# Optimization experiments

Hardware: AMD Instinct MI355X
Metric: run time of the kernel (lower is better)

The kernel has to match this reference:

```python
import jax, jax.numpy as jnp
import numpy as np

HW, B, C, NH, NC, HF, WF = 2500, 2, 256, 8, 6, 64, 176
DFF = 4 * C
EPS = 1e-5

def _layernorm(x, g, b):
    m = x.mean(-1, keepdims=True)
    v = ((x - m) ** 2).mean(-1, keepdims=True)
    return (x - m) / jnp.sqrt(v + EPS) * g + b

def _mha(q, kv, in_w, in_b, ow, ob):
    # q: [L,B,C], kv: [S,B,C] (batch_first=False, torch nn.MultiheadAttention)
    L, Bq, Cq = q.shape
    S = kv.shape[0]
    Dh = Cq // NH
    qp = (q @ in_w[:Cq].T + in_b[:Cq]).reshape(L, Bq, NH, Dh)
    kp = (kv @ in_w[Cq:2 * Cq].T + in_b[Cq:2 * Cq]).reshape(S, Bq, NH, Dh)
    vp = (kv @ in_w[2 * Cq:].T + in_b[2 * Cq:]).reshape(S, Bq, NH, Dh)
    att = jnp.einsum('lbhd,sbhd->bhls', qp, kp) * (1.0 / np.sqrt(Dh))
    att = jax.nn.softmax(att, axis=-1)
    out = jnp.einsum('bhls,sbhd->lbhd', att, vp).reshape(L, Bq, Cq)
    return out @ ow.T + ob

def _grid_sample_zeros(feat, grid):
    # feat: [B,N,C,H,W], grid: [B,N,Q,2] in [-1,1]; bilinear, align_corners=False, zero padding
    Bb, N, Cc, Hf, Wf = feat.shape
    Q = grid.shape[2]
    x = (grid[..., 0] + 1.0) * (Wf / 2.0) - 0.5
    y = (grid[..., 1] + 1.0) * (Hf / 2.0) - 0.5
    x0 = jnp.floor(x); y0 = jnp.floor(y)
    wx = x - x0; wy = y - y0
    x0i = x0.astype(jnp.int32); y0i = y0.astype(jnp.int32)
    ff = feat.reshape(Bb, N, Cc, Hf * Wf)
    def corner(xi, yi, w):
        valid = (xi >= 0) & (xi < Wf) & (yi >= 0) & (yi < Hf)
        idx = jnp.clip(yi, 0, Hf - 1) * Wf + jnp.clip(xi, 0, Wf - 1)  # [B,N,Q]
        g = jnp.take_along_axis(ff, jnp.broadcast_to(idx[:, :, None, :], (Bb, N, Cc, Q)), axis=-1)
        return g * (w * valid)[:, :, None, :]
    return (corner(x0i, y0i, (1.0 - wx) * (1.0 - wy)) + corner(x0i + 1, y0i, wx * (1.0 - wy))
            + corner(x0i, y0i + 1, (1.0 - wx) * wy) + corner(x0i + 1, y0i + 1, wx * wy))

def _forward(bev_queries, prev_bev, image_feat, reference_points, camera_intrinsics, camera_extrinsics,
             in_proj_w, in_proj_b, out_proj_w, out_proj_b, tsa_norm_g, tsa_norm_b,
             sca_w, sca_b, sca_norm_g, sca_norm_b, ffn_w1, ffn_b1, ffn_w2, ffn_b2, ffn_norm_g, ffn_norm_b):
    # TSA (dropout is identity in eval)
    tsa_out = _mha(bev_queries, prev_bev, in_proj_w, in_proj_b, out_proj_w, out_proj_b)
    x = _layernorm(bev_queries + tsa_out, tsa_norm_g, tsa_norm_b)
    # SCA: ego->camera->image projection
    R = camera_extrinsics[:, :, :3, :3]            # [B,N,3,3]
    t = camera_extrinsics[:, :, :3, 3]             # [B,N,3]
    R_e2c = jnp.swapaxes(R, -1, -2)
    t_e2c = -jnp.einsum('bnij,bnj->bni', R_e2c, t)
    pts_cam = jnp.einsum('bnij,qj->bnqi', R_e2c, reference_points) + t_e2c[:, :, None, :]  # [B,N,Q,3]
    pts_img = jnp.einsum('bnij,bnqj->bnqi', camera_intrinsics, pts_cam)
    uv = pts_img[..., :2] / jnp.maximum(pts_img[..., 2:3], 1e-5)
    grid = jnp.stack([2.0 * uv[..., 0] / WF - 1.0, 2.0 * uv[..., 1] / HF - 1.0], axis=-1)  # [B,N,Q,2]
    Bq = bev_queries.shape[1]
    feat_r = image_feat.reshape(Bq, NC, C, HF, WF)
    sampled = _grid_sample_zeros(feat_r, grid).mean(axis=1)   # [B,C,Q]
    sampled = jnp.transpose(sampled, (2, 0, 1))               # [Q,B,C]
    sca_out = sampled @ sca_w.T + sca_b
    x = _layernorm(x + sca_out, sca_norm_g, sca_norm_b)
    # FFN (torch nn.GELU default = exact erf)
    h = jax.nn.gelu(x @ ffn_w1 + ffn_b1, approximate=False)
    ffn_out = h @ ffn_w2 + ffn_b2
    return _layernorm(x + ffn_out, ffn_norm_g, ffn_norm_b)

def setup_inputs():
    key = jax.random.key(0)
    ks = jax.random.split(key, 16)
    f = jnp.float32
    s = 0.02
    return {
        'bev_queries': jax.random.normal(ks[0], (HW, B, C), f),
        'prev_bev': jax.random.normal(ks[1], (HW, B, C), f),
        'image_feat': jax.random.normal(ks[2], (B * NC, C, HF, WF), f),
        'reference_points': jax.random.normal(ks[3], (HW, 3), f) * 20.0,
        'camera_intrinsics': jax.random.normal(ks[4], (B, NC, 3, 3), f),
        'camera_extrinsics': jax.random.normal(ks[5], (B, NC, 4, 4), f),
        'spatial_shapes': jnp.array([[HF, WF]], jnp.int32),
        'in_proj_w': jax.random.normal(ks[6], (3 * C, C), f) * s,
        'in_proj_b': jnp.zeros((3 * C,), f),
        'out_proj_w': jax.random.normal(ks[7], (C, C), f) * s,
        'out_proj_b': jnp.zeros((C,), f),
        'tsa_norm_g': jnp.ones((C,), f), 'tsa_norm_b': jnp.zeros((C,), f),
        'sca_w': jax.random.normal(ks[8], (C, C), f) * s,
        'sca_b': jnp.zeros((C,), f),
        'sca_norm_g': jnp.ones((C,), f), 'sca_norm_b': jnp.zeros((C,), f),
        'ffn_w1': jax.random.normal(ks[9], (C, DFF), f) * s,
        'ffn_b1': jnp.zeros((DFF,), f),
        'ffn_w2': jax.random.normal(ks[10], (DFF, C), f) * s,
        'ffn_b2': jnp.zeros((C,), f),
        'ffn_norm_g': jnp.ones((C,), f), 'ffn_norm_b': jnp.zeros((C,), f),
    }

def reference(bev_queries, prev_bev, image_feat, reference_points, camera_intrinsics, camera_extrinsics,
              in_proj_w, in_proj_b, out_proj_w, out_proj_b, tsa_norm_g, tsa_norm_b,
              sca_w, sca_b, sca_norm_g, sca_norm_b, ffn_w1, ffn_b1, ffn_w2, ffn_b2, ffn_norm_g, ffn_norm_b,
              spatial_shapes):
    return _forward(bev_queries, prev_bev, image_feat, reference_points, camera_intrinsics, camera_extrinsics,
                    in_proj_w, in_proj_b, out_proj_w, out_proj_b, tsa_norm_g, tsa_norm_b,
                    sca_w, sca_b, sca_norm_g, sca_norm_b, ffn_w1, ffn_b1, ffn_w2, ffn_b2, ffn_norm_g, ffn_norm_b)
```

## Files before the change

kernel.cpp:

```cpp
#include <hip/hip_runtime.h>

typedef unsigned short u16;
typedef __attribute__((ext_vector_type(8))) __bf16 bf8_t;
typedef __attribute__((ext_vector_type(4))) float f4_t;

union bf8u { u16 u[8]; bf8_t v; uint4 q; };

__device__ __forceinline__ float bf2f(u16 v) {
  return __uint_as_float(((unsigned int)v) << 16);
}
__device__ __forceinline__ u16 f2bf(float f) {
  union { __bf16 h; u16 u; } c;
  c.h = (__bf16)f;
  return c.u;
}
__device__ __forceinline__ float bflo(unsigned int w) { return __uint_as_float(w << 16); }
__device__ __forceinline__ float bfhi(unsigned int w) { return __uint_as_float(w & 0xFFFF0000u); }
__device__ __forceinline__ float ldf1(const void* p, size_t i, int isf32) {
  return isf32 ? ((const float*)p)[i] : bf2f(((const u16*)p)[i]);
}

#define LQ    2500
#define LQP   2560
#define BB    2
#define CC    256
#define NCC   6
#define HFF   64
#define WFF   176
#define DFF   1024
#define MROWS 5000

#define WB_UV   256
#define WB_WQKV 240256
#define WB_WOP  633472
#define WB_WSC  764544
#define WB_WF1  895616
#define WB_WF2  1419904
#define WB_S1   1944192
#define WB_S2   (WB_S1 + 2621440)
#define WB_S3   (WB_S2 + 2621440)
#define WB_VT   (WB_S3 + 2621440)
#define WB_H    WB_S2
#define WB_Y3   (WB_S2 + 10485760)

__global__ void detect_k(const u16* __restrict__ rp, int* __restrict__ flag) {
  int bad = 0;
  for (int i = threadIdx.x; i < 7500; i += 64) {
    float v = bf2f(rp[i]);
    if (!(fabsf(v) < 1e6f)) bad = 1;
  }
  int anybad = __any(bad);
  if (threadIdx.x == 0) flag[0] = anybad ? 1 : 0;
}

struct WDesc {
  const void* src[6];
  u16* dst[6];
  int n[6];
  int mode[6];
  int Kd[6], Nd[6];
};
__global__ __launch_bounds__(256) void cvtw_k(WDesc d, const int* __restrict__ flag) {
  const int df = flag[0];
  const int i = blockIdx.y;
  const int n = d.n[i];
  for (int j = blockIdx.x * 256 + threadIdx.x; j < n; j += gridDim.x * 256) {
    if (d.mode[i] == 2) {
      const int row = j / (LQP - LQ), col = LQ + j % (LQP - LQ);
      d.dst[i][(size_t)row * LQP + col] = 0;
    } else if (d.mode[i] == 1) {
      const int K = d.Kd[i], N = d.Nd[i];
      const int nn = j / K, kk = j - nn * K;
      d.dst[i][j] = f2bf(ldf1(d.src[i], (size_t)kk * N + nn, df));
    } else {
      d.dst[i][j] = f2bf(ldf1(d.src[i], j, df));
    }
  }
}

template<int KTPL, int XRAW, int ACT, int RES, int STORE_T, int NT>
__global__ __launch_bounds__(64) void gemm_nl(
    const void* __restrict__ Xv, const u16* __restrict__ W,
    const void* __restrict__ bias, size_t boff,
    const void* __restrict__ resv,
    u16* __restrict__ Y, int M, int N, const int* __restrict__ flag)
{
  const int df = flag[0];
  const int lane = threadIdx.x;
  const int ln15 = lane & 15, l4 = lane >> 4;
  const int m0 = blockIdx.x * 16, n0 = blockIdx.y * (NT * 16);
  const int am = min(m0 + ln15, M - 1);

  f4_t acc[NT];
#pragma unroll
  for (int nt = 0; nt < NT; ++nt) acc[nt] = (f4_t){0.f, 0.f, 0.f, 0.f};

#pragma unroll 8
  for (int k0 = 0; k0 < KTPL; k0 += 32) {
    bf8u a;
    if (XRAW && df) {
      const float* p = (const float*)Xv + (size_t)am * KTPL + k0 + l4 * 8;
      float4 r0 = *(const float4*)p, r1 = *(const float4*)(p + 4);
      a.u[0]=f2bf(r0.x); a.u[1]=f2bf(r0.y); a.u[2]=f2bf(r0.z); a.u[3]=f2bf(r0.w);
      a.u[4]=f2bf(r1.x); a.u[5]=f2bf(r1.y); a.u[6]=f2bf(r1.z); a.u[7]=f2bf(r1.w);
    } else {
      a.q = *(const uint4*)((const u16*)Xv + (size_t)am * KTPL + k0 + l4 * 8);
    }
#pragma unroll
    for (int nt = 0; nt < NT; ++nt) {
      bf8u b;
      b.q = *(const uint4*)&W[(size_t)(n0 + nt * 16 + ln15) * KTPL + k0 + l4 * 8];
      acc[nt] = __builtin_amdgcn_mfma_f32_16x16x32_bf16(a.v, b.v, acc[nt], 0, 0, 0);
    }
  }
#pragma unroll
  for (int nt = 0; nt < NT; ++nt) {
    const int gn = n0 + nt * 16 + ln15;
    const float bv = ldf1(bias, boff + gn, df);
#pragma unroll
    for (int r = 0; r < 4; ++r) {
      const int gm = m0 + l4 * 4 + r;
      if (gm < M) {
        float x = acc[nt][r] + bv;
        if (ACT) x = 0.5f * x * (1.f + erff(x * 0.70710678118654752f));
        if (RES == 1)      x += bf2f(((const u16*)resv)[(size_t)gm * N + gn]);
        else if (RES == 2) x += ldf1(resv, (size_t)gm * N + gn, df);
        if (STORE_T) {
          const int tt = gm >> 1;
          const int tx = tt & 63;
          const int tp = (tx & 35) | ((tx & 12) << 1) | ((tx & 16) >> 2);
          Y[(size_t)(gn + (gm & 1) * 256) * LQP + ((tt & ~63) | tp)] = f2bf(x);
        } else {
          Y[(size_t)gm * N + gn] = f2bf(x);
        }
      }
    }
  }
}

__global__ __launch_bounds__(64) void gemm_qkv(
    const void* __restrict__ Xq, const void* __restrict__ Xkv,
    const u16* __restrict__ Wqkv, const void* __restrict__ bias,
    u16* __restrict__ Qo, u16* __restrict__ Ko, u16* __restrict__ Vt,
    const int* __restrict__ flag)
{
  const int df = flag[0];
  const int lane = threadIdx.x;
  const int ln15 = lane & 15, l4 = lane >> 4;
  const int which = blockIdx.y >> 2;
  const int n0 = (blockIdx.y & 3) * 64;
  const void* Xv = (which == 0) ? Xq : Xkv;
  const u16* W = Wqkv + (size_t)which * 65536;
  const int m0 = blockIdx.x * 16;
  const int am = min(m0 + ln15, MROWS - 1);

  f4_t acc[4];
#pragma unroll
  for (int nt = 0; nt < 4; ++nt) acc[nt] = (f4_t){0.f, 0.f, 0.f, 0.f};

#pragma unroll 8
  for (int k0 = 0; k0 < CC; k0 += 32) {
    bf8u a;
    if (df) {
      const float* p = (const float*)Xv + (size_t)am * CC + k0 + l4 * 8;
      float4 r0 = *(const float4*)p, r1 = *(const float4*)(p + 4);
      a.u[0]=f2bf(r0.x); a.u[1]=f2bf(r0.y); a.u[2]=f2bf(r0.z); a.u[3]=f2bf(r0.w);
      a.u[4]=f2bf(r1.x); a.u[5]=f2bf(r1.y); a.u[6]=f2bf(r1.z); a.u[7]=f2bf(r1.w);
    } else {
      a.q = *(const uint4*)((const u16*)Xv + (size_t)am * CC + k0 + l4 * 8);
    }
#pragma unroll
    for (int nt = 0; nt < 4; ++nt) {
      bf8u b;
      b.q = *(const uint4*)&W[(size_t)(n0 + nt * 16 + ln15) * CC + k0 + l4 * 8];
      acc[nt] = __builtin_amdgcn_mfma_f32_16x16x32_bf16(a.v, b.v, acc[nt], 0, 0, 0);
    }
  }
#pragma unroll
  for (int nt = 0; nt < 4; ++nt) {
    const int gn = n0 + nt * 16 + ln15;
    const float bv = ldf1(bias, which * 256 + gn, df);
#pragma unroll
    for (int r = 0; r < 4; ++r) {
      const int gm = m0 + l4 * 4 + r;
      if (gm < MROWS) {
        const float x = acc[nt][r] + bv;
        if (which == 2) {
          const int tt = gm >> 1;
          const int tx = tt & 63;
          const int tp = (tx & 35) | ((tx & 12) << 1) | ((tx & 16) >> 2);
          Vt[(size_t)(gn + (gm & 1) * 256) * LQP + ((tt & ~63) | tp)] = f2bf(x);
        } else {
          u16* Y = (which == 0) ? Qo : Ko;
          Y[(size_t)gm * CC + gn] = f2bf(x);
        }
      }
    }
  }
}

#define TPW 10
__global__ __launch_bounds__(256) void attn_mf(
    const u16* __restrict__ Qw, const u16* __restrict__ Kw,
    const u16* __restrict__ Vt, u16* __restrict__ Ow)
{
  __shared__ float sO[4][16][33];
  __shared__ float sM[4][16];
  __shared__ float sL[4][16];
  const int t = threadIdx.x;
  const int lane = t & 63, w = t >> 6;
  const int ln15 = lane & 15, l4 = lane >> 4;
  const int q0 = blockIdx.x * 16;
  const int by = blockIdx.y;
  const int b = by >> 3, h = by & 7;
  const float SCL2E = 0.25505654481f;

  bf8u aq;
  {
    const int qrow = min(q0 + ln15, LQ - 1);
    bf8u qr; qr.q = *(const uint4*)&Qw[((size_t)qrow * BB + b) * CC + h * 32 + l4 * 8];
#pragma unroll
    for (int i = 0; i < 8; ++i) aq.u[i] = f2bf(bf2f(qr.u[i]) * SCL2E);
  }

  f4_t oacc[2];
  oacc[0] = (f4_t){0.f,0.f,0.f,0.f};
  oacc[1] = (f4_t){0.f,0.f,0.f,0.f};
  float m_r = -1e30f;
  float l_r = 0.f;

  const int kt0 = w * TPW;
  const u16* Kbase = &Kw[(size_t)b * CC + h * 32 + l4 * 8];
  const u16* Vbase = &Vt[(size_t)(by * 32 + ln15) * LQP + l4 * 8];

  bf8u bkn[4];
#pragma unroll
  for (int nt = 0; nt < 4; ++nt)
    bkn[nt].q = *(const uint4*)&Kbase[(size_t)(kt0 * 64 + nt * 16 + ln15) * CC];

  for (int kt = kt0; kt < kt0 + TPW; ++kt) {
    const int kb = kt * 64;
    bf8u av[2][2];
#pragma unroll
    for (int m = 0; m < 2; ++m)
#pragma unroll
      for (int dt = 0; dt < 2; ++dt)
        av[m][dt].q = *(const uint4*)&Vbase[(size_t)(dt * 16) * LQP + kb + m * 32];
    bf8u bk[4];
#pragma unroll
    for (int nt = 0; nt < 4; ++nt) bk[nt] = bkn[nt];
    if (kt + 1 < kt0 + TPW) {
#pragma unroll
      for (int nt = 0; nt < 4; ++nt)
        bkn[nt].q = *(const uint4*)&Kbase[(size_t)(kb + 64 + nt * 16 + ln15) * CC];
    }
    f4_t sv[4];
    __builtin_amdgcn_s_setprio(1);
#pragma unroll
    for (int nt = 0; nt < 4; ++nt) {
      f4_t z = (f4_t){0.f,0.f,0.f,0.f};
      sv[nt] = __builtin_amdgcn_mfma_f32_16x16x32_bf16(bk[nt].v, aq.v, z, 0, 0, 0);
    }
    __builtin_amdgcn_s_setprio(0);
    float p[4][4];
    if (kb + 64 <= LQ) {
#pragma unroll
      for (int nt = 0; nt < 4; ++nt)
#pragma unroll
        for (int r = 0; r < 4; ++r) p[nt][r] = sv[nt][r];
    } else {
#pragma unroll
      for (int nt = 0; nt < 4; ++nt)
#pragma unroll
        for (int r = 0; r < 4; ++r)
          p[nt][r] = (kb + nt * 16 + l4 * 4 + r < LQ) ? sv[nt][r] : -1e30f;
    }
    const float m0 = fmaxf(fmaxf(p[0][0], p[0][1]), fmaxf(p[0][2], p[0][3]));
    const float m1 = fmaxf(fmaxf(p[1][0], p[1][1]), fmaxf(p[1][2], p[1][3]));
    const float m2 = fmaxf(fmaxf(p[2][0], p[2][1]), fmaxf(p[2][2], p[2][3]));
    const float m3 = fmaxf(fmaxf(p[3][0], p[3][1]), fmaxf(p[3][2], p[3][3]));
    float mloc = fmaxf(fmaxf(m0, m1), fmaxf(m2, m3));
    mloc = fmaxf(mloc, __shfl_xor(mloc, 16));
    mloc = fmaxf(mloc, __shfl_xor(mloc, 32));
    if (__any(mloc > m_r + 8.f)) {
      const float mn = fmaxf(m_r, mloc);
      const float alpha = __builtin_amdgcn_exp2f(m_r - mn);
      m_r = mn;
      l_r *= alpha;
#pragma unroll
      for (int r = 0; r < 4; ++r) { oacc[0][r] *= alpha; oacc[1][r] *= alpha; }
    }
    float s = 0.f;
#pragma unroll
    for (int nt = 0; nt < 4; ++nt) {
#pragma unroll
      for (int r = 0; r < 4; ++r) {
        const float e = __builtin_amdgcn_exp2f(p[nt][r] - m_r);
        p[nt][r] = e; s += e;
      }
    }
    l_r += s;
    __builtin_amdgcn_s_setprio(1);
#pragma unroll
    for (int m = 0; m < 2; ++m) {
      bf8u pb;
#pragma unroll
      for (int i = 0; i < 8; ++i) pb.u[i] = f2bf(p[2 * m + (i >> 2)][i & 3]);
#pragma unroll
      for (int dt = 0; dt < 2; ++dt)
        oacc[dt] = __builtin_amdgcn_mfma_f32_16x16x32_bf16(av[m][dt].v, pb.v, oacc[dt], 0, 0, 0);
    }
    __builtin_amdgcn_s_setprio(0);
  }
  l_r += __shfl_xor(l_r, 16);
  l_r += __shfl_xor(l_r, 32);
#pragma unroll
  for (int dt = 0; dt < 2; ++dt)
#pragma unroll
    for (int r = 0; r < 4; ++r)
      sO[w][ln15][dt * 16 + l4 * 4 + r] = oacc[dt][r];
  if (l4 == 0) { sM[w][ln15] = m_r; sL[w][ln15] = l_r; }
  __syncthreads();
#pragma unroll
  for (int i = t; i < 512; i += 256) {
    const int row = i >> 5, col = i & 31;
    const float M = fmaxf(fmaxf(sM[0][row], sM[1][row]), fmaxf(sM[2][row], sM[3][row]));
    float l = 0.f, O = 0.f;
#pragma unroll
    for (int w4 = 0; w4 < 4; ++w4) {
      const float sc = __builtin_amdgcn_exp2f(sM[w4][row] - M);
      l += sc * sL[w4][row];
      O += sc * sO[w4][row][col];
    }
    const int q = q0 + row;
    if (q < LQ)
      Ow[((size_t)q * BB + b) * CC + h * 32 + col] = f2bf(O / l);
  }
}

template<int TOOUT>
__global__ __launch_bounds__(256) void ln_k(const u16* __restrict__ X,
    const void* __restrict__ g, const void* __restrict__ be,
    void* __restrict__ Yv, int rows, const int* __restrict__ flag)
{
  const int df = flag[0];
  const int lane = threadIdx.x & 63;
  const int row = blockIdx.x * 4 + (threadIdx.x >> 6);
  if (row >= rows) return;
  uint2 raw = *(const uint2*)(X + (size_t)row * CC + lane * 4);
  float vx = bflo(raw.x), vy = bfhi(raw.x), vz = bflo(raw.y), vw = bfhi(raw.y);
  float s = vx + vy + vz + vw;
#pragma unroll
  for (int o = 1; o < 64; o <<= 1) s += __shfl_xor(s, o);
  const float mean = s * 0.00390625f;
  const float dx = vx - mean, dy = vy - mean, dz = vz - mean, dw = vw - mean;
  float sq = dx*dx + dy*dy + dz*dz + dw*dw;
#pragma unroll
  for (int o = 1; o < 64; o <<= 1) sq += __shfl_xor(sq, o);
  const float rstd = rsqrtf(sq * 0.00390625f + 1e-5f);
  const float g0 = ldf1(g, lane*4+0, df), g1 = ldf1(g, lane*4+1, df);
  const float g2 = ldf1(g, lane*4+2, df), g3 = ldf1(g, lane*4+3, df);
  const float b0 = ldf1(be, lane*4+0, df), b1 = ldf1(be, lane*4+1, df);
  const float b2 = ldf1(be, lane*4+2, df), b3 = ldf1(be, lane*4+3, df);
  const float y0 = dx * rstd * g0 + b0;
  const float y1 = dy * rstd * g1 + b1;
  const float y2 = dz * rstd * g2 + b2;
  const float y3 = dw * rstd * g3 + b3;
  if (TOOUT && df) {
    float* yp = (float*)Yv + (size_t)row * CC + lane * 4;
    *(float4*)yp = make_float4(y0, y1, y2, y3);
  } else {
    u16* yp = (u16*)Yv + (size_t)row * CC + lane * 4;
    unsigned int lo = (unsigned int)f2bf(y0) | ((unsigned int)f2bf(y1) << 16);
    unsigned int hi = (unsigned int)f2bf(y2) | ((unsigned int)f2bf(y3) << 16);
    *(uint2*)yp = make_uint2(lo, hi);
  }
}

__global__ __launch_bounds__(256) void uv_k(
    const void* __restrict__ refp, const void* __restrict__ intr,
    const void* __restrict__ extr, float* __restrict__ uv,
    const int* __restrict__ flag)
{
  const int df = flag[0];
  const int idx = blockIdx.x * 256 + threadIdx.x;
  if (idx >= BB * NCC * LQ) return;
  const int bc = idx / LQ;
  const int q = idx - bc * LQ;
  float R[3][3], tv[3], Kc[3][3], p[3];
#pragma unroll
  for (int i = 0; i < 3; ++i) {
#pragma unroll
    for (int j = 0; j < 3; ++j) {
      R[i][j] = ldf1(extr, bc*16 + i*4 + j, df);
      Kc[i][j] = ldf1(intr, bc*9 + i*3 + j, df);
    }
    tv[i] = ldf1(extr, bc*16 + i*4 + 3, df);
  }
#pragma unroll
  for (int j = 0; j < 3; ++j) p[j] = ldf1(refp, q*3 + j, df) - tv[j];
  float pc[3];
#pragma unroll
  for (int i = 0; i < 3; ++i) pc[i] = R[0][i]*p[0] + R[1][i]*p[1] + R[2][i]*p[2];
  float im[3];
#pragma unroll
  for (int i = 0; i < 3; ++i) im[i] = Kc[i][0]*pc[0] + Kc[i][1]*pc[1] + Kc[i][2]*pc[2];
  const float z = fmaxf(im[2], 1e-5f);
  uv[(size_t)idx*2 + 0] = im[0] / z - 0.5f;
  uv[(size_t)idx*2 + 1] = im[1] / z - 0.5f;
}

__global__ __launch_bounds__(256) void samp_k(
    const void* __restrict__ feat, const float* __restrict__ uv,
    u16* __restrict__ S, const int* __restrict__ flag)
{
  const int df = flag[0];
  const int c = blockIdx.x;
  const int b = blockIdx.y / 5;
  const int ch = blockIdx.y % 5;
  const int qend = min((ch + 1) * 500, LQ);
  for (int q = ch * 500 + threadIdx.x; q < qend; q += 256) {
    float acc = 0.f;
#pragma unroll
    for (int cam = 0; cam < NCC; ++cam) {
      const int bc = b * NCC + cam;
      const float x = uv[((size_t)bc * LQ + q) * 2 + 0];
      const float y = uv[((size_t)bc * LQ + q) * 2 + 1];
      const float xf = floorf(x), yf = floorf(y);
      const int x0 = (int)xf, y0 = (int)yf;
      const float wx = x - xf, wy = y - yf;
      const size_t base = ((size_t)bc * CC + c) * (HFF * WFF);
      const bool vx0 = (x0 >= 0) & (x0 < WFF);
      const bool vx1 = (x0 + 1 >= 0) & (x0 + 1 < WFF);
      const bool vy0 = (y0 >= 0) & (y0 < HFF);
      const bool vy1 = (y0 + 1 >= 0) & (y0 + 1 < HFF);
      if (vy0) {
        const size_t rb = base + (size_t)y0 * WFF;
        if (vx0) acc += (1.f - wx) * (1.f - wy) * ldf1(feat, rb + x0, df);
        if (vx1) acc += wx * (1.f - wy) * ldf1(feat, rb + x0 + 1, df);
      }
      if (vy1) {
        const size_t rb = base + (size_t)(y0 + 1) * WFF;
        if (vx0) acc += (1.f - wx) * wy * ldf1(feat, rb + x0, df);
        if (vx1) acc += wx * wy * ldf1(feat, rb + x0 + 1, df);
      }
    }
    S[((size_t)q * BB + b) * CC + c] = f2bf(acc * (1.f / 6.f));
  }
}

extern "C" void kernel_launch(void* const* d_in, const int* in_sizes, int n_in,
                              void* d_out, int out_size, void* d_ws, size_t ws_size,
                              hipStream_t stream) {
  (void)in_sizes; (void)n_in; (void)out_size; (void)ws_size;
  char* base = (char*)d_ws;
  int* flag = (int*)base;
  float* UV = (float*)(base + WB_UV);
  u16* WQKV = (u16*)(base + WB_WQKV);
  u16* WOP  = (u16*)(base + WB_WOP);
  u16* WSC  = (u16*)(base + WB_WSC);
  u16* WF1  = (u16*)(base + WB_WF1);
  u16* WF2  = (u16*)(base + WB_WF2);
  u16* S1 = (u16*)(base + WB_S1);
  u16* S2 = (u16*)(base + WB_S2);
  u16* S3 = (u16*)(base + WB_S3);
  u16* VT = (u16*)(base + WB_VT);
  u16* H  = (u16*)(base + WB_H);
  u16* Y3 = (u16*)(base + WB_Y3);

  detect_k<<<1, 64, 0, stream>>>((const u16*)d_in[3], flag);

  WDesc wd;
  wd.src[0] = d_in[7];  wd.dst[0] = WQKV; wd.n[0] = 196608; wd.mode[0] = 0; wd.Kd[0] = 0;    wd.Nd[0] = 0;
  wd.src[1] = d_in[9];  wd.dst[1] = WOP;  wd.n[1] = 65536;  wd.mode[1] = 0; wd.Kd[1] = 0;    wd.Nd[1] = 0;
  wd.src[2] = d_in[13]; wd.dst[2] = WSC;  wd.n[2] = 65536;  wd.mode[2] = 0; wd.Kd[2] = 0;    wd.Nd[2] = 0;
  wd.src[3] = d_in[17]; wd.dst[3] = WF1;  wd.n[3] = 262144; wd.mode[3] = 1; wd.Kd[3] = 256;  wd.Nd[3] = 1024;
  wd.src[4] = d_in[19]; wd.dst[4] = WF2;  wd.n[4] = 262144; wd.mode[4] = 1; wd.Kd[4] = 1024; wd.Nd[4] = 256;
  wd.src[5] = nullptr;  wd.dst[5] = VT;   wd.n[5] = 512 * (LQP - LQ); wd.mode[5] = 2; wd.Kd[5] = 0; wd.Nd[5] = 0;
  cvtw_k<<<dim3(128, 6), 256, 0, stream>>>(wd, flag);

  uv_k<<<(BB * NCC * LQ + 255) / 256, 256, 0, stream>>>(d_in[3], d_in[4], d_in[5], UV, flag);

  gemm_qkv<<<dim3(313, 12), 64, 0, stream>>>(d_in[0], d_in[1], WQKV, d_in[8], S1, S2, VT, flag);

  attn_mf<<<dim3(157, 16), 256, 0, stream>>>(S1, S2, VT, S3);

  gemm_nl<256,0,0,2,0,1><<<dim3(313, 16), 64, 0, stream>>>(S3, WOP, d_in[10], 0, d_in[0], S1, MROWS, CC, flag);
  ln_k<0><<<1250, 256, 0, stream>>>(S1, d_in[11], d_in[12], S2, MROWS, flag);

  samp_k<<<dim3(CC, BB * 5), 256, 0, stream>>>(d_in[2], UV, VT, flag);

  gemm_nl<256,0,0,1,0,1><<<dim3(313, 16), 64, 0, stream>>>(VT, WSC, d_in[14], 0, S2, S3, MROWS, CC, flag);
  ln_k<0><<<1250, 256, 0, stream>>>(S3, d_in[15], d_in[16], S1, MROWS, flag);

  gemm_nl<256,0,1,0,0,4><<<dim3(313, 16), 64, 0, stream>>>(S1, WF1, d_in[18], 0, nullptr, H,  MROWS, DFF, flag);
  gemm_nl<1024,0,0,1,0,1><<<dim3(313, 16), 64, 0, stream>>>(H,  WF2, d_in[20], 0, S1,      Y3, MROWS, CC,  flag);
  ln_k<1><<<1250, 256, 0, stream>>>(Y3, d_in[21], d_in[22], d_out, MROWS, flag);
}
```

Baseline: 519.7 us.

## Stage camera feature planes in LDS for sampling and widen GEMM N-tiles

The sampling kernel now loads each 64x176 feature plane for a (channel, camera) into shared memory, converting bf16 to float once, then samples all queries from LDS. Each thread keeps ten per-query accumulators across the six cameras, so the grid drops from 10 to 2 blocks per channel. This removes scattered global gathers at the cost of 44KB of LDS per block and lower occupancy. Three N=256 GEMMs also switch to a template setting that covers four times as many output columns per block, cutting grid.y from 16 to 4.

```diff
diff --git a/kernel.cpp b/kernel.cpp
--- a/kernel.cpp
+++ b/kernel.cpp
@@ -414,38 +414,71 @@
     const void* __restrict__ feat, const float* __restrict__ uv,
     u16* __restrict__ S, const int* __restrict__ flag)
 {
+  __shared__ float pl[HFF * WFF];
   const int df = flag[0];
   const int c = blockIdx.x;
-  const int b = blockIdx.y / 5;
-  const int ch = blockIdx.y % 5;
-  const int qend = min((ch + 1) * 500, LQ);
-  for (int q = ch * 500 + threadIdx.x; q < qend; q += 256) {
-    float acc = 0.f;
-#pragma unroll
-    for (int cam = 0; cam < NCC; ++cam) {
-      const int bc = b * NCC + cam;
-      const float x = uv[((size_t)bc * LQ + q) * 2 + 0];
-      const float y = uv[((size_t)bc * LQ + q) * 2 + 1];
-      const float xf = floorf(x), yf = floorf(y);
-      const int x0 = (int)xf, y0 = (int)yf;
-      const float wx = x - xf, wy = y - yf;
-      const size_t base = ((size_t)bc * CC + c) * (HFF * WFF);
-      const bool vx0 = (x0 >= 0) & (x0 < WFF);
-      const bool vx1 = (x0 + 1 >= 0) & (x0 + 1 < WFF);
-      const bool vy0 = (y0 >= 0) & (y0 < HFF);
-      const bool vy1 = (y0 + 1 >= 0) & (y0 + 1 < HFF);
-      if (vy0) {
-        const size_t rb = base + (size_t)y0 * WFF;
-        if (vx0) acc += (1.f - wx) * (1.f - wy) * ldf1(feat, rb + x0, df);
-        if (vx1) acc += wx * (1.f - wy) * ldf1(feat, rb + x0 + 1, df);
+  const int b = blockIdx.y;
+  const int t = threadIdx.x;
+
+  float acc[10];
+#pragma unroll
+  for (int j = 0; j < 10; ++j) acc[j] = 0.f;
+
+  for (int cam = 0; cam < NCC; ++cam) {
+    const int bc = b * NCC + cam;
+    const size_t base = ((size_t)bc * CC + c) * (HFF * WFF);
+    __syncthreads();
+    if (df) {
+      const float4* src = (const float4*)((const float*)feat + base);
+#pragma unroll
+      for (int i = 0; i < 11; ++i) {
+        const int g = i * 256 + t;
+        *(float4*)&pl[g * 4] = src[g];
       }
-      if (vy1) {
-        const size_t rb = base + (size_t)(y0 + 1) * WFF;
-        if (vx0) acc += (1.f - wx) * wy * ldf1(feat, rb + x0, df);
-        if (vx1) acc += wx * wy * ldf1(feat, rb + x0 + 1, df);
+    } else {
+      const uint2* src = (const uint2*)((const u16*)feat + base);
+#pragma unroll
+      for (int i = 0; i < 11; ++i) {
+        const int g = i * 256 + t;
+        const uint2 r = src[g];
+        *(float4*)&pl[g * 4] = make_float4(bflo(r.x), bfhi(r.x), bflo(r.y), bfhi(r.y));
       }
     }
-    S[((size_t)q * BB + b) * CC + c] = f2bf(acc * (1.f / 6.f));
+    __syncthreads();
+    const float* uvb = &uv[(size_t)bc * LQ * 2];
+#pragma unroll
+    for (int j = 0; j < 10; ++j) {
+      const int q = j * 256 + t;
+      if (q < LQ) {
+        const float x = uvb[q * 2 + 0];
+        const float y = uvb[q * 2 + 1];
+        const float xf = floorf(x), yf = floorf(y);
+        const int x0 = (int)xf, y0 = (int)yf;
+        const float wx = x - xf, wy = y - yf;
+        const bool vx0 = (x0 >= 0) & (x0 < WFF);
+        const bool vx1 = (x0 + 1 >= 0) & (x0 + 1 < WFF);
+        const bool vy0 = (y0 >= 0) & (y0 < HFF);
+        const bool vy1 = (y0 + 1 >= 0) & (y0 + 1 < HFF);
+        float a = 0.f;
+        if (vy0) {
+          const int rb = y0 * WFF;
+          if (vx0) a += (1.f - wx) * (1.f - wy) * pl[rb + x0];
+          if (vx1) a += wx * (1.f - wy) * pl[rb + x0 + 1];
+        }
+        if (vy1) {
+          const int rb = (y0 + 1) * WFF;
+          if (vx0) a += (1.f - wx) * wy * pl[rb + x0];
+          if (vx1) a += wx * wy * pl[rb + x0 + 1];
+        }
+        acc[j] += a;
+      }
+    }
+  }
+#pragma unroll
+  for (int j = 0; j < 10; ++j) {
+    const int q = j * 256 + t;
+    if (q < LQ)
+      S[((size_t)q * BB + b) * CC + c] = f2bf(acc[j] * (1.f / 6.f));
   }
 }
 
@@ -485,15 +518,15 @@
 
   attn_mf<<<dim3(157, 16), 256, 0, stream>>>(S1, S2, VT, S3);
 
-  gemm_nl<256,0,0,2,0,1><<<dim3(313, 16), 64, 0, stream>>>(S3, WOP, d_in[10], 0, d_in[0], S1, MROWS, CC, flag);
+  gemm_nl<256,0,0,2,0,4><<<dim3(313, 4), 64, 0, stream>>>(S3, WOP, d_in[10], 0, d_in[0], S1, MROWS, CC, flag);
   ln_k<0><<<1250, 256, 0, stream>>>(S1, d_in[11], d_in[12], S2, MROWS, flag);
 
-  samp_k<<<dim3(CC, BB * 5), 256, 0, stream>>>(d_in[2], UV, VT, flag);
-
-  gemm_nl<256,0,0,1,0,1><<<dim3(313, 16), 64, 0, stream>>>(VT, WSC, d_in[14], 0, S2, S3, MROWS, CC, flag);
+  samp_k<<<dim3(CC, BB), 256, 0, stream>>>(d_in[2], UV, VT, flag);
+
+  gemm_nl<256,0,0,1,0,4><<<dim3(313, 4), 64, 0, stream>>>(VT, WSC, d_in[14], 0, S2, S3, MROWS, CC, flag);
   ln_k<0><<<1250, 256, 0, stream>>>(S3, d_in[15], d_in[16], S1, MROWS, flag);
 
   gemm_nl<256,0,1,0,0,4><<<dim3(313, 16), 64, 0, stream>>>(S1, WF1, d_in[18], 0, nullptr, H,  MROWS, DFF, flag);
-  gemm_nl<1024,0,0,1,0,1><<<dim3(313, 16), 64, 0, stream>>>(H,  WF2, d_in[20], 0, S1,      Y3, MROWS, CC,  flag);
+  gemm_nl<1024,0,0,1,0,4><<<dim3(313, 4),  64, 0, stream>>>(H,  WF2, d_in[20], 0, S1,      Y3, MROWS, CC,  flag);
   ln_k<1><<<1250, 256, 0, stream>>>(Y3, d_in[21], d_in[22], d_out, MROWS, flag);
 }
```

Measured after the change: 517.0 us. No clear change (-0.5%).

## Fuse layernorm into output GEMMs, merge uv projection into weight conversion

Applied to the files above, without the earlier changes.

Adds a gemm_ln kernel in which four waves each compute 64 output columns of a 16-row tile, add bias and residual, and apply layernorm through shared-memory row reductions. It replaces three GEMM plus ln_k pairs, which removes three launches and the write and re-read of the pre-norm intermediates. The uv camera projection now runs as an extra grid row of the weight conversion kernel, the plain weight copies are vectorised to four elements per thread, and the attention rescale check skips the max reduction when no element passes the threshold. A cost is that each output GEMM now launches 313 blocks instead of 5008, which lowers parallelism across CUs.

```diff
diff --git a/kernel.cpp b/kernel.cpp
--- a/kernel.cpp
+++ b/kernel.cpp
@@ -41,7 +41,6 @@
 #define WB_S3   (WB_S2 + 2621440)
 #define WB_VT   (WB_S3 + 2621440)
 #define WB_H    WB_S2
-#define WB_Y3   (WB_S2 + 10485760)
 
 __global__ void detect_k(const u16* __restrict__ rp, int* __restrict__ flag) {
   int bad = 0;
@@ -60,29 +59,66 @@
   int mode[6];
   int Kd[6], Nd[6];
 };
-__global__ __launch_bounds__(256) void cvtw_k(WDesc d, const int* __restrict__ flag) {
+__global__ __launch_bounds__(256) void cvtw_k(WDesc d,
+    const void* __restrict__ refp, const void* __restrict__ intr,
+    const void* __restrict__ extr, float* __restrict__ uv,
+    const int* __restrict__ flag) {
   const int df = flag[0];
   const int i = blockIdx.y;
+  if (i == 6) {
+    for (int idx = blockIdx.x * 256 + threadIdx.x; idx < BB * NCC * LQ; idx += gridDim.x * 256) {
+      const int bc = idx / LQ;
+      const int q = idx - bc * LQ;
+      float R[3][3], tv[3], Kc[3][3], p[3];
+#pragma unroll
+      for (int a = 0; a < 3; ++a) {
+#pragma unroll
+        for (int j = 0; j < 3; ++j) {
+          R[a][j] = ldf1(extr, bc*16 + a*4 + j, df);
+          Kc[a][j] = ldf1(intr, bc*9 + a*3 + j, df);
+        }
+        tv[a] = ldf1(extr, bc*16 + a*4 + 3, df);
+      }
+#pragma unroll
+      for (int j = 0; j < 3; ++j) p[j] = ldf1(refp, q*3 + j, df) - tv[j];
+      float pc[3];
+#pragma unroll
+      for (int a = 0; a < 3; ++a) pc[a] = R[0][a]*p[0] + R[1][a]*p[1] + R[2][a]*p[2];
+      float im[3];
+#pragma unroll
+      for (int a = 0; a < 3; ++a) im[a] = Kc[a][0]*pc[0] + Kc[a][1]*pc[1] + Kc[a][2]*pc[2];
+      const float z = fmaxf(im[2], 1e-5f);
+      uv[(size_t)idx*2 + 0] = im[0] / z - 0.5f;
+      uv[(size_t)idx*2 + 1] = im[1] / z - 0.5f;
+    }
+    return;
+  }
   const int n = d.n[i];
   for (int j = blockIdx.x * 256 + threadIdx.x; j < n; j += gridDim.x * 256) {
-    if (d.mode[i] == 2) {
+    if (d.mode[i] == 3) {
+      if (df) {
+        const float4 r = ((const float4*)d.src[i])[j];
+        const unsigned int lo = (unsigned int)f2bf(r.x) | ((unsigned int)f2bf(r.y) << 16);
+        const unsigned int hi = (unsigned int)f2bf(r.z) | ((unsigned int)f2bf(r.w) << 16);
+        ((uint2*)d.dst[i])[j] = make_uint2(lo, hi);
+      } else {
+        ((uint2*)d.dst[i])[j] = ((const uint2*)d.src[i])[j];
+      }
+    } else if (d.mode[i] == 2) {
       const int row = j / (LQP - LQ), col = LQ + j % (LQP - LQ);
       d.dst[i][(size_t)row * LQP + col] = 0;
-    } else if (d.mode[i] == 1) {
+    } else {
       const int K = d.Kd[i], N = d.Nd[i];
       const int nn = j / K, kk = j - nn * K;
       d.dst[i][j] = f2bf(ldf1(d.src[i], (size_t)kk * N + nn, df));
-    } else {
-      d.dst[i][j] = f2bf(ldf1(d.src[i], j, df));
-    }
-  }
-}
-
-template<int KTPL, int XRAW, int ACT, int RES, int STORE_T, int NT>
+    }
+  }
+}
+
+template<int KTPL, int ACT, int NT>
 __global__ __launch_bounds__(64) void gemm_nl(
-    const void* __restrict__ Xv, const u16* __restrict__ W,
-    const void* __restrict__ bias, size_t boff,
-    const void* __restrict__ resv,
+    const u16* __restrict__ Xv, const u16* __restrict__ W,
+    const void* __restrict__ bias,
     u16* __restrict__ Y, int M, int N, const int* __restrict__ flag)
 {
   const int df = flag[0];
@@ -98,14 +134,7 @@
 #pragma unroll 8
   for (int k0 = 0; k0 < KTPL; k0 += 32) {
     bf8u a;
-    if (XRAW && df) {
-      const float* p = (const float*)Xv + (size_t)am * KTPL + k0 + l4 * 8;
-      float4 r0 = *(const float4*)p, r1 = *(const float4*)(p + 4);
-      a.u[0]=f2bf(r0.x); a.u[1]=f2bf(r0.y); a.u[2]=f2bf(r0.z); a.u[3]=f2bf(r0.w);
-      a.u[4]=f2bf(r1.x); a.u[5]=f2bf(r1.y); a.u[6]=f2bf(r1.z); a.u[7]=f2bf(r1.w);
-    } else {
-      a.q = *(const uint4*)((const u16*)Xv + (size_t)am * KTPL + k0 + l4 * 8);
-    }
+    a.q = *(const uint4*)(Xv + (size_t)am * KTPL + k0 + l4 * 8);
 #pragma unroll
     for (int nt = 0; nt < NT; ++nt) {
       bf8u b;
@@ -116,23 +145,116 @@
 #pragma unroll
   for (int nt = 0; nt < NT; ++nt) {
     const int gn = n0 + nt * 16 + ln15;
-    const float bv = ldf1(bias, boff + gn, df);
+    const float bv = ldf1(bias, gn, df);
 #pragma unroll
     for (int r = 0; r < 4; ++r) {
       const int gm = m0 + l4 * 4 + r;
       if (gm < M) {
         float x = acc[nt][r] + bv;
         if (ACT) x = 0.5f * x * (1.f + erff(x * 0.70710678118654752f));
-        if (RES == 1)      x += bf2f(((const u16*)resv)[(size_t)gm * N + gn]);
-        else if (RES == 2) x += ldf1(resv, (size_t)gm * N + gn, df);
-        if (STORE_T) {
-          const int tt = gm >> 1;
-          const int tx = tt & 63;
-          const int tp = (tx & 35) | ((tx & 12) << 1) | ((tx & 16) >> 2);
-          Y[(size_t)(gn + (gm & 1) * 256) * LQP + ((tt & ~63) | tp)] = f2bf(x);
-        } else {
-          Y[(size_t)gm * N + gn] = f2bf(x);
-        }
+        Y[(size_t)gm * N + gn] = f2bf(x);
+      }
+    }
+  }
+}
+
+template<int KT, int RES, int TOOUT>
+__global__ __launch_bounds__(256) void gemm_ln(
+    const u16* __restrict__ Xv, const u16* __restrict__ W,
+    const void* __restrict__ bias, const void* __restrict__ resv,
+    const void* __restrict__ gw, const void* __restrict__ bw,
+    void* __restrict__ Yv, int M, const int* __restrict__ flag)
+{
+  __shared__ float sR[4][16];
+  const int df = flag[0];
+  const int t = threadIdx.x;
+  const int lane = t & 63, wn = t >> 6;
+  const int ln15 = lane & 15, l4 = lane >> 4;
+  const int m0 = blockIdx.x * 16;
+  const int am = min(m0 + ln15, M - 1);
+
+  f4_t acc[4];
+#pragma unroll
+  for (int nt = 0; nt < 4; ++nt) acc[nt] = (f4_t){0.f, 0.f, 0.f, 0.f};
+
+#pragma unroll 8
+  for (int k0 = 0; k0 < KT; k0 += 32) {
+    bf8u a;
+    a.q = *(const uint4*)(Xv + (size_t)am * KT + k0 + l4 * 8);
+#pragma unroll
+    for (int nt = 0; nt < 4; ++nt) {
+      bf8u b;
+      b.q = *(const uint4*)&W[(size_t)(wn * 64 + nt * 16 + ln15) * KT + k0 + l4 * 8];
+      acc[nt] = __builtin_amdgcn_mfma_f32_16x16x32_bf16(a.v, b.v, acc[nt], 0, 0, 0);
+    }
+  }
+  float x[4][4];
+#pragma unroll
+  for (int nt = 0; nt < 4; ++nt) {
+    const int gn = wn * 64 + nt * 16 + ln15;
+    const float bv = ldf1(bias, gn, df);
+#pragma unroll
+    for (int r = 0; r < 4; ++r) {
+      const int gm = m0 + l4 * 4 + r;
+      float xx = acc[nt][r] + bv;
+      const size_t ri = (size_t)min(gm, M - 1) * CC + gn;
+      if (RES == 1)      xx += bf2f(((const u16*)resv)[ri]);
+      else if (RES == 2) xx += ldf1(resv, ri, df);
+      x[nt][r] = xx;
+    }
+  }
+  float ps[4];
+#pragma unroll
+  for (int r = 0; r < 4; ++r) {
+    ps[r] = x[0][r] + x[1][r] + x[2][r] + x[3][r];
+#pragma unroll
+    for (int o = 1; o < 16; o <<= 1) ps[r] += __shfl_xor(ps[r], o);
+  }
+  if (ln15 == 0) {
+#pragma unroll
+    for (int r = 0; r < 4; ++r) sR[wn][l4 * 4 + r] = ps[r];
+  }
+  __syncthreads();
+  float mean[4];
+#pragma unroll
+  for (int r = 0; r < 4; ++r) {
+    const int row = l4 * 4 + r;
+    mean[r] = (sR[0][row] + sR[1][row] + sR[2][row] + sR[3][row]) * 0.00390625f;
+  }
+  __syncthreads();
+  float pq[4];
+#pragma unroll
+  for (int r = 0; r < 4; ++r) {
+    float d0 = x[0][r] - mean[r], d1 = x[1][r] - mean[r];
+    float d2 = x[2][r] - mean[r], d3 = x[3][r] - mean[r];
+    pq[r] = d0*d0 + d1*d1 + d2*d2 + d3*d3;
+#pragma unroll
+    for (int o = 1; o < 16; o <<= 1) pq[r] += __shfl_xor(pq[r], o);
+  }
+  if (ln15 == 0) {
+#pragma unroll
+    for (int r = 0; r < 4; ++r) sR[wn][l4 * 4 + r] = pq[r];
+  }
+  __syncthreads();
+  float rstd[4];
+#pragma unroll
+  for (int r = 0; r < 4; ++r) {
+    const int row = l4 * 4 + r;
+    const float v = (sR[0][row] + sR[1][row] + sR[2][row] + sR[3][row]) * 0.00390625f;
+    rstd[r] = rsqrtf(v + 1e-5f);
+  }
+#pragma unroll
+  for (int nt = 0; nt < 4; ++nt) {
+    const int gn = wn * 64 + nt * 16 + ln15;
+    const float g = ldf1(gw, gn, df);
+    const float be = ldf1(bw, gn, df);
+#pragma unroll
+    for (int r = 0; r < 4; ++r) {
+      const int gm = m0 + l4 * 4 + r;
+      if (gm < M) {
+        const float y = (x[nt][r] - mean[r]) * rstd[r] * g + be;
+        if (TOOUT && df) ((float*)Yv)[(size_t)gm * CC + gn] = y;
+        else             ((u16*)Yv)[(size_t)gm * CC + gn] = f2bf(y);
       }
     }
   }
@@ -275,14 +397,20 @@
         for (int r = 0; r < 4; ++r)
           p[nt][r] = (kb + nt * 16 + l4 * 4 + r < LQ) ? sv[nt][r] : -1e30f;
     }
-    const float m0 = fmaxf(fmaxf(p[0][0], p[0][1]), fmaxf(p[0][2], p[0][3]));
-    const float m1 = fmaxf(fmaxf(p[1][0], p[1][1]), fmaxf(p[1][2], p[1][3]));
-    const float m2 = fmaxf(fmaxf(p[2][0], p[2][1]), fmaxf(p[2][2], p[2][3]));
-    const float m3 = fmaxf(fmaxf(p[3][0], p[3][1]), fmaxf(p[3][2], p[3][3]));
-    float mloc = fmaxf(fmaxf(m0, m1), fmaxf(m2, m3));
-    mloc = fmaxf(mloc, __shfl_xor(mloc, 16));
-    mloc = fmaxf(mloc, __shfl_xor(mloc, 32));
-    if (__any(mloc > m_r + 8.f)) {
+    const float thr = m_r + 8.f;
+    bool nd = false;
+#pragma unroll
+    for (int nt = 0; nt < 4; ++nt)
+#pragma unroll
+      for (int r = 0; r < 4; ++r) nd |= (p[nt][r] > thr);
+    if (__any(nd)) {
+      const float m0 = fmaxf(fmaxf(p[0][0], p[0][1]), fmaxf(p[0][2], p[0][3]));
+      const float m1 = fmaxf(fmaxf(p[1][0], p[1][1]), fmaxf(p[1][2], p[1][3]));
+      const float m2 = fmaxf(fmaxf(p[2][0], p[2][1]), fmaxf(p[2][2], p[2][3]));
+      const float m3 = fmaxf(fmaxf(p[3][0], p[3][1]), fmaxf(p[3][2], p[3][3]));
+      float mloc = fmaxf(fmaxf(m0, m1), fmaxf(m2, m3));
+      mloc = fmaxf(mloc, __shfl_xor(mloc, 16));
+      mloc = fmaxf(mloc, __shfl_xor(mloc, 32));
       const float mn = fmaxf(m_r, mloc);
       const float alpha = __builtin_amdgcn_exp2f(m_r - mn);
       m_r = mn;
@@ -336,78 +464,6 @@
     if (q < LQ)
       Ow[((size_t)q * BB + b) * CC + h * 32 + col] = f2bf(O / l);
   }
-}
-
-template<int TOOUT>
-__global__ __launch_bounds__(256) void ln_k(const u16* __restrict__ X,
-    const void* __restrict__ g, const void* __restrict__ be,
-    void* __restrict__ Yv, int rows, const int* __restrict__ flag)
-{
-  const int df = flag[0];
-  const int lane = threadIdx.x & 63;
-  const int row = blockIdx.x * 4 + (threadIdx.x >> 6);
-  if (row >= rows) return;
-  uint2 raw = *(const uint2*)(X + (size_t)row * CC + lane * 4);
-  float vx = bflo(raw.x), vy = bfhi(raw.x), vz = bflo(raw.y), vw = bfhi(raw.y);
-  float s = vx + vy + vz + vw;
-#pragma unroll
-  for (int o = 1; o < 64; o <<= 1) s += __shfl_xor(s, o);
-  const float mean = s * 0.00390625f;
-  const float dx = vx - mean, dy = vy - mean, dz = vz - mean, dw = vw - mean;
-  float sq = dx*dx + dy*dy + dz*dz + dw*dw;
-#pragma unroll
-  for (int o = 1; o < 64; o <<= 1) sq += __shfl_xor(sq, o);
-  const float rstd = rsqrtf(sq * 0.00390625f + 1e-5f);
-  const float g0 = ldf1(g, lane*4+0, df), g1 = ldf1(g, lane*4+1, df);
-  const float g2 = ldf1(g, lane*4+2, df), g3 = ldf1(g, lane*4+3, df);
-  const float b0 = ldf1(be, lane*4+0, df), b1 = ldf1(be, lane*4+1, df);
-  const float b2 = ldf1(be, lane*4+2, df), b3 = ldf1(be, lane*4+3, df);
-  const float y0 = dx * rstd * g0 + b0;
-  const float y1 = dy * rstd * g1 + b1;
-  const float y2 = dz * rstd * g2 + b2;
-  const float y3 = dw * rstd * g3 + b3;
-  if (TOOUT && df) {
-    float* yp = (float*)Yv + (size_t)row * CC + lane * 4;
-    *(float4*)yp = make_float4(y0, y1, y2, y3);
-  } else {
-    u16* yp = (u16*)Yv + (size_t)row * CC + lane * 4;
-    unsigned int lo = (unsigned int)f2bf(y0) | ((unsigned int)f2bf(y1) << 16);
-    unsigned int hi = (unsigned int)f2bf(y2) | ((unsigned int)f2bf(y3) << 16);
-    *(uint2*)yp = make_uint2(lo, hi);
-  }
-}
-
-__global__ __launch_bounds__(256) void uv_k(
-    const void* __restrict__ refp, const void* __restrict__ intr,
-    const void* __restrict__ extr, float* __restrict__ uv,
-    const int* __restrict__ flag)
-{
-  const int df = flag[0];
-  const int idx = blockIdx.x * 256 + threadIdx.x;
-  if (idx >= BB * NCC * LQ) return;
-  const int bc = idx / LQ;
-  const int q = idx - bc * LQ;
-  float R[3][3], tv[3], Kc[3][3], p[3];
-#pragma unroll
-  for (int i = 0; i < 3; ++i) {
-#pragma unroll
-    for (int j = 0; j < 3; ++j) {
-      R[i][j] = ldf1(extr, bc*16 + i*4 + j, df);
-      Kc[i][j] = ldf1(intr, bc*9 + i*3 + j, df);
-    }
-    tv[i] = ldf1(extr, bc*16 + i*4 + 3, df);
-  }
-#pragma unroll
-  for (int j = 0; j < 3; ++j) p[j] = ldf1(refp, q*3 + j, df) - tv[j];
-  float pc[3];
-#pragma unroll
-  for (int i = 0; i < 3; ++i) pc[i] = R[0][i]*p[0] + R[1][i]*p[1] + R[2][i]*p[2];
-  float im[3];
-#pragma unroll
-  for (int i = 0; i < 3; ++i) im[i] = Kc[i][0]*pc[0] + Kc[i][1]*pc[1] + Kc[i][2]*pc[2];
-  const float z = fmaxf(im[2], 1e-5f);
-  uv[(size_t)idx*2 + 0] = im[0] / z - 0.5f;
-  uv[(size_t)idx*2 + 1] = im[1] / z - 0.5f;
 }
 
 __global__ __launch_bounds__(256) void samp_k(
@@ -466,34 +522,28 @@
   u16* S3 = (u16*)(base + WB_S3);
   u16* VT = (u16*)(base + WB_VT);
   u16* H  = (u16*)(base + WB_H);
-  u16* Y3 = (u16*)(base + WB_Y3);
 
   detect_k<<<1, 64, 0, stream>>>((const u16*)d_in[3], flag);
 
   WDesc wd;
-  wd.src[0] = d_in[7];  wd.dst[0] = WQKV; wd.n[0] = 196608; wd.mode[0] = 0; wd.Kd[0] = 0;    wd.Nd[0] = 0;
-  wd.src[1] = d_in[9];  wd.dst[1] = WOP;  wd.n[1] = 65536;  wd.mode[1] = 0; wd.Kd[1] = 0;    wd.Nd[1] = 0;
-  wd.src[2] = d_in[13]; wd.dst[2] = WSC;  wd.n[2] = 65536;  wd.mode[2] = 0; wd.Kd[2] = 0;    wd.Nd[2] = 0;
+  wd.src[0] = d_in[7];  wd.dst[0] = WQKV; wd.n[0] = 49152;  wd.mode[0] = 3; wd.Kd[0] = 0;    wd.Nd[0] = 0;
+  wd.src[1] = d_in[9];  wd.dst[1] = WOP;  wd.n[1] = 16384;  wd.mode[1] = 3; wd.Kd[1] = 0;    wd.Nd[1] = 0;
+  wd.src[2] = d_in[13]; wd.dst[2] = WSC;  wd.n[2] = 16384;  wd.mode[2] = 3; wd.Kd[2] = 0;    wd.Nd[2] = 0;
   wd.src[3] = d_in[17]; wd.dst[3] = WF1;  wd.n[3] = 262144; wd.mode[3] = 1; wd.Kd[3] = 256;  wd.Nd[3] = 1024;
   wd.src[4] = d_in[19]; wd.dst[4] = WF2;  wd.n[4] = 262144; wd.mode[4] = 1; wd.Kd[4] = 1024; wd.Nd[4] = 256;
   wd.src[5] = nullptr;  wd.dst[5] = VT;   wd.n[5] = 512 * (LQP - LQ); wd.mode[5] = 2; wd.Kd[5] = 0; wd.Nd[5] = 0;
-  cvtw_k<<<dim3(128, 6), 256, 0, stream>>>(wd, flag);
-
-  uv_k<<<(BB * NCC * LQ + 255) / 256, 256, 0, stream>>>(d_in[3], d_in[4], d_in[5], UV, flag);
+  cvtw_k<<<dim3(128, 7), 256, 0, stream>>>(wd, d_in[3], d_in[4], d_in[5], UV, flag);
 
   gemm_qkv<<<dim3(313, 12), 64, 0, stream>>>(d_in[0], d_in[1], WQKV, d_in[8], S1, S2, VT, flag);
 
   attn_mf<<<dim3(157, 16), 256, 0, stream>>>(S1, S2, VT, S3);
 
-  gemm_nl<256,0,0,2,0,1><<<dim3(313, 16), 64, 0, stream>>>(S3, WOP, d_in[10], 0, d_in[0], S1, MROWS, CC, flag);
-  ln_k<0><<<1250, 256, 0, stream>>>(S1, d_in[11], d_in[12], S2, MROWS, flag);
+  gemm_ln<256,2,0><<<313, 256, 0, stream>>>(S3, WOP, d_in[10], d_in[0], d_in[11], d_in[12], S2, MROWS, flag);
 
   samp_k<<<dim3(CC, BB * 5), 256, 0, stream>>>(d_in[2], UV, VT, flag);
 
-  gemm_nl<256,0,0,1,0,1><<<dim3(313, 16), 64, 0, stream>>>(VT, WSC, d_in[14], 0, S2, S3, MROWS, CC, flag);
-  ln_k<0><<<1250, 256, 0, stream>>>(S3, d_in[15], d_in[16], S1, MROWS, flag);
-
-  gemm_nl<256,0,1,0,0,4><<<dim3(313, 16), 64, 0, stream>>>(S1, WF1, d_in[18], 0, nullptr, H,  MROWS, DFF, flag);
-  gemm_nl<1024,0,0,1,0,1><<<dim3(313, 16), 64, 0, stream>>>(H,  WF2, d_in[20], 0, S1,      Y3, MROWS, CC,  flag);
-  ln_k<1><<<1250, 256, 0, stream>>>(Y3, d_in[21], d_in[22], d_out, MROWS, flag);
-}
+  gemm_ln<256,1,0><<<313, 256, 0, stream>>>(VT, WSC, d_in[14], S2, d_in[15], d_in[16], S1, MROWS, flag);
+
+  gemm_nl<256,1,4><<<dim3(313, 16), 64, 0, stream>>>(S1, WF1, d_in[18], H, MROWS, DFF, flag);
+  gemm_ln<1024,1,1><<<313, 256, 0, stream>>>(H, WF2, d_in[20], S1, d_in[21], d_in[22], d_out, MROWS, flag);
+}
```

Result: faster. 503.7 us (-3.1%).
